# Performance work log

Measured on AMD Instinct MI355X. Metric: run time of the kernel, lower is better.

The kernel has to match this reference:

```python
import jax, jax.numpy as jnp
import numpy as np

S, B, H = 4096, 1, 2048       # [seq, batch, hidden] layout (NeoX convention)
NP, HN = 16, H // 16          # heads, head dim
ROT = int(HN * 0.25)          # rotary_ndims = 32 (rotary_pct=0.25)
ROPE_BASE = 10000.0


def setup_inputs() -> dict:
    key = jax.random.key(0)
    k0, k1, k2 = jax.random.split(key, 3)
    hidden_states = jax.random.normal(k0, (S, B, H), jnp.float32) * 0.02
    # causal left-to-right mask: True = masked out (filled with -10000)
    attention_mask = jnp.triu(jnp.ones((1, 1, S, S), bool), k=1)
    w_qkv = jax.random.normal(k1, (3 * H, H), jnp.float32) * (1.0 / np.sqrt(H))
    w_dense = jax.random.normal(k2, (H, H), jnp.float32) * (1.0 / np.sqrt(H))
    b_dense = jnp.zeros((H,), jnp.float32)
    return {"hidden_states": hidden_states, "attention_mask": attention_mask,
            "w_qkv": w_qkv, "w_dense": w_dense, "b_dense": b_dense}


def _apply_rope(x, pos):
    # x: [s, b, np, ROT]; NeoX rotate_half convention
    inv_freq = 1.0 / (ROPE_BASE ** (jnp.arange(0, ROT, 2, dtype=jnp.float32) / ROT))
    freqs = pos[:, None] * inv_freq[None, :]              # [s, ROT/2]
    emb = jnp.concatenate([freqs, freqs], axis=-1)        # [s, ROT]
    cos = jnp.cos(emb)[:, None, None, :]
    sin = jnp.sin(emb)[:, None, None, :]
    x1, x2 = jnp.split(x, 2, axis=-1)
    rot = jnp.concatenate([-x2, x1], axis=-1)
    return x * cos + rot * sin


def reference(hidden_states, attention_mask, w_qkv, w_dense, b_dense):
    s, b, h = hidden_states.shape
    # fused QKV projection (no bias), reshape to [s, b, np, 3*hn], split
    qkv = (hidden_states @ w_qkv.T).reshape(s, b, NP, 3 * HN)
    q, k, v = jnp.split(qkv, 3, axis=-1)                  # each [s, b, np, hn]
    # partial rotary embedding on first ROT dims
    pos = jnp.arange(s, dtype=jnp.float32)
    q = jnp.concatenate([_apply_rope(q[..., :ROT], pos), q[..., ROT:]], axis=-1)
    k = jnp.concatenate([_apply_rope(k[..., :ROT], pos), k[..., ROT:]], axis=-1)
    # raw attention scores [b, np, s_q, s_k], scale 1/sqrt(hn)
    scores = jnp.einsum('sbhd,tbhd->bhst', q, k) / np.float32(np.sqrt(HN))
    # ltor mask: fill masked positions with -10000, softmax in fp32
    scores = jnp.where(attention_mask, jnp.float32(-10000.0), scores)
    probs = jax.nn.softmax(scores.astype(jnp.float32), axis=-1).astype(hidden_states.dtype)
    # context [s, b, np, hn] -> [s, b, h]
    ctx = jnp.einsum('bhst,tbhd->sbhd', probs, v).reshape(s, b, h)
    return ctx @ w_dense.T + b_dense
```

## Files before the change

### kernel.cpp

```cpp
#include <hip/hip_runtime.h>

#define S_LEN 4096
#define HID   2048
#define NHEAD 16
#define HDIM  128
#define QSCALE_L2E 0.12751664352f

typedef float  f32x4  __attribute__((ext_vector_type(4)));
typedef float  f32x16 __attribute__((ext_vector_type(16)));
typedef __bf16 bf16x8 __attribute__((ext_vector_type(8)));
typedef unsigned u32x4 __attribute__((ext_vector_type(4)));
typedef unsigned u32x2 __attribute__((ext_vector_type(2)));

#define MFMA16(a, b, c) __builtin_amdgcn_mfma_f32_16x16x32_bf16((a), (b), (c), 0, 0, 0)
#define MFMA32(a, b, c) __builtin_amdgcn_mfma_f32_32x32x16_bf16((a), (b), (c), 0, 0, 0)

__device__ __forceinline__ void gld16(const void* g, void* l) {
  __builtin_amdgcn_global_load_lds(
      (const __attribute__((address_space(1))) void*)(unsigned long long)(g),
      (__attribute__((address_space(3))) void*)(unsigned long long)(l),
      16, 0, 0);
}

__device__ __forceinline__ unsigned short f2bf(float f) {
  union { float f; unsigned u; } v; v.f = f;
  unsigned r = v.u + 0x7FFFu + ((v.u >> 16) & 1u);
  return (unsigned short)(r >> 16);
}
__device__ __forceinline__ float bf2f(unsigned short h) {
  union { unsigned u; float f; } v; v.u = ((unsigned)h) << 16;
  return v.f;
}
__device__ __forceinline__ unsigned cvtpk_bf16(float a, float b) {
  unsigned r;
  asm("v_cvt_pk_bf16_f32 %0, %1, %2" : "=v"(r) : "v"(a), "v"(b));
  return r;
}
__device__ __forceinline__ u32x2 pls(unsigned a, unsigned b) {
  return __builtin_amdgcn_permlane32_swap(a, b, false, false);
}
__device__ __forceinline__ float asf(unsigned u) { return __builtin_bit_cast(float, u); }
__device__ __forceinline__ unsigned asu(float f) { return __builtin_bit_cast(unsigned, f); }

__global__ __launch_bounds__(256) void cvt_kernel(const float* __restrict__ src,
                                                  unsigned short* __restrict__ dst, int n) {
  int i = (blockIdx.x * 256 + threadIdx.x) * 4;
  if (i >= n) return;
  const float4 v = *(const float4*)(src + i);
  ushort4 o;
  o.x = f2bf(v.x); o.y = f2bf(v.y); o.z = f2bf(v.z); o.w = f2bf(v.w);
  *(ushort4*)(dst + i) = o;
}

__global__ __launch_bounds__(256, 3) void gemm_qkv_kernel(
    const unsigned short* __restrict__ A, const unsigned short* __restrict__ B,
    unsigned short* __restrict__ Qb, unsigned short* __restrict__ Kb,
    unsigned short* __restrict__ Vt) {
  __shared__ __align__(16) unsigned short As[2][128 * 32];
  __shared__ __align__(16) unsigned short Bs[2][128 * 32];
  const int K = HID;
  const int bid = ((int)blockIdx.x % 8) * 192 + (int)blockIdx.x / 8;
  const int bm = bid / 48, bn = bid % 48;
  const int row0 = bm * 128, col0 = bn * 128;
  const int tid = threadIdx.x;
  const int wid = tid >> 6, lane = tid & 63;
  const int g = lane >> 4, r16 = lane & 15;
  const int wr = wid >> 1, wc = wid & 1;

  f32x4 acc[4][4] = {};

  int srow[2], scol[2];
#pragma unroll
  for (int c = 0; c < 2; ++c) {
    int byteoff = (wid * 2 + c) * 1024 + lane * 16;
    srow[c] = byteoff >> 6;
    scol[c] = (byteoff & 63) >> 1;
  }

  auto stage = [&](int buf, int t) {
    const int k0 = t * 32;
#pragma unroll
    for (int c = 0; c < 2; ++c) {
      gld16(A + (row0 + srow[c]) * K + k0 + scol[c], &As[buf][(wid * 2 + c) * 512]);
      gld16(B + (col0 + srow[c]) * K + k0 + scol[c], &Bs[buf][(wid * 2 + c) * 512]);
    }
  };

  const int nt = K / 32;
  stage(0, 0);
  __syncthreads();
  for (int t = 0; t < nt; ++t) {
    const int cur = t & 1;
    if (t + 1 < nt) stage(cur ^ 1, t + 1);
    const char* as = (const char*)As[cur];
    const char* bs = (const char*)Bs[cur];
    bf16x8 af[4], bfv[4];
#pragma unroll
    for (int m = 0; m < 4; ++m)
      af[m] = *(const bf16x8*)(as + (wr * 64 + m * 16 + r16) * 64 + g * 16);
#pragma unroll
    for (int n = 0; n < 4; ++n)
      bfv[n] = *(const bf16x8*)(bs + (wc * 64 + n * 16 + r16) * 64 + g * 16);
#pragma unroll
    for (int m = 0; m < 4; ++m)
#pragma unroll
      for (int n = 0; n < 4; ++n)
        acc[m][n] = MFMA16(af[m], bfv[n], acc[m][n]);
    __syncthreads();
  }

  const int type = bn % 3, p = bn / 3;
#pragma unroll
  for (int m = 0; m < 4; ++m) {
    const int s0 = row0 + wr * 64 + m * 16 + g * 4;
#pragma unroll
    for (int n = 0; n < 4; ++n) {
      const int d = wc * 64 + n * 16 + r16;
      if (type == 0) {
#pragma unroll
        for (int r = 0; r < 4; ++r)
          Qb[(p * S_LEN + s0 + r) * HDIM + d] = f2bf(acc[m][n][r] * QSCALE_L2E);
      } else if (type == 1) {
#pragma unroll
        for (int r = 0; r < 4; ++r)
          Kb[(p * S_LEN + s0 + r) * HDIM + d] = f2bf(acc[m][n][r]);
      } else {
        ushort4 o;
        o.x = f2bf(acc[m][n][0]); o.y = f2bf(acc[m][n][1]);
        o.z = f2bf(acc[m][n][2]); o.w = f2bf(acc[m][n][3]);
        *(ushort4*)(Vt + (p * HDIM + d) * S_LEN + s0) = o;
      }
    }
  }
}

__global__ __launch_bounds__(256) void rope_kernel(unsigned short* __restrict__ Qb,
                                                   unsigned short* __restrict__ Kb) {
  const int idx = blockIdx.x * 256 + threadIdx.x;
  const int p = idx >> 16, rem = idx & 65535, s = rem >> 4, d = rem & 15;
  const float invf = exp2f(-(float)d * (13.287712379549449f / 16.0f));
  const float ang = (float)s * invf;
  const float c = cosf(ang), sn = sinf(ang);
  const int base = (p * S_LEN + s) * HDIM;
  {
    float x = bf2f(Qb[base + d]), y = bf2f(Qb[base + d + 16]);
    Qb[base + d]      = f2bf(x * c - y * sn);
    Qb[base + d + 16] = f2bf(y * c + x * sn);
  }
  {
    float x = bf2f(Kb[base + d]), y = bf2f(Kb[base + d + 16]);
    Kb[base + d]      = f2bf(x * c - y * sn);
    Kb[base + d + 16] = f2bf(y * c + x * sn);
  }
}

__global__ __launch_bounds__(256, 2) void attn_kernel(
    const unsigned short* __restrict__ Qb, const unsigned short* __restrict__ Kb,
    const unsigned short* __restrict__ Vt, unsigned short* __restrict__ Ctx) {
  __shared__ __align__(16) unsigned char sm[65536];
  unsigned char* const Kl0 = sm;
  unsigned char* const Vl0 = sm + 32768;
  const int b = (int)blockIdx.x;
  const int p = b & 15;
  const int qt = (b < 256) ? (b >> 4) : 47 - (b >> 4);
  const int tid = threadIdx.x, wid = tid >> 6, lane = tid & 63;
  const int l31 = lane & 31, hi = lane >> 5;
  const int xr = (l31 & 7) << 4;

  auto stageKV = [&](int buf, int t) {
    const unsigned short* kb = Kb + (p * S_LEN + t * 64) * HDIM;
    const unsigned short* vb = Vt + p * HDIM * S_LEN + t * 64;
#pragma unroll
    for (int c = 0; c < 4; ++c) {
      const int chunk = c * 256 + tid;
      const int byteoff = chunk * 16;
      {
        const int j = byteoff >> 8, cb = (byteoff >> 4) & 15;
        gld16(kb + j * HDIM + (cb ^ (j & 7)) * 8, Kl0 + buf * 16384 + chunk * 16);
      }
      {
        const int dd = byteoff >> 7, cb = (byteoff >> 4) & 7;
        gld16(vb + dd * S_LEN + (cb ^ (dd & 7)) * 8, Vl0 + buf * 16384 + chunk * 16);
      }
    }
  };

  const int q0w = qt * 128 + wid * 32;
  const int qg = q0w + l31;
  const int nt = 2 * (qt + 1);

  stageKV(0, 0);
  bf16x8 qf[8];
  {
    const unsigned short* qp_ = Qb + (p * S_LEN + qg) * HDIM + hi * 8;
#pragma unroll
    for (int dd = 0; dd < 8; ++dd) qf[dd] = *(const bf16x8*)(qp_ + dd * 16);
  }
  f32x16 acc[4] = {};
  float m_s = -1e30f, l_s = 0.f;

  __syncthreads();
  for (int t = 0; t < nt; ++t) {
    const int cur = t & 1;
    if (t + 1 < nt) stageKV(cur ^ 1, t + 1);
    const unsigned char* kl = Kl0 + cur * 16384;
    const unsigned char* vl = Vl0 + cur * 16384;

    f32x16 sv0 = {}, sv1 = {};
    __builtin_amdgcn_s_setprio(1);
#pragma unroll
    for (int dd = 0; dd < 8; ++dd) {
      bf16x8 k0 = *(const bf16x8*)(kl + l31 * 256 + (((dd * 2 + hi) << 4) ^ xr));
      bf16x8 k1 = *(const bf16x8*)(kl + (32 + l31) * 256 + (((dd * 2 + hi) << 4) ^ xr));
      sv0 = MFMA32(k0, qf[dd], sv0);
      sv1 = MFMA32(k1, qf[dd], sv1);
    }
    __builtin_amdgcn_s_setprio(0);
    if (t * 64 + 63 > q0w) {
#pragma unroll
      for (int r = 0; r < 16; ++r) {
        const int kv0 = t * 64 + ((r & 3) + 8 * (r >> 2)) + 4 * hi;
        if (kv0 > qg) sv0[r] = -1e30f;
        if (kv0 + 32 > qg) sv1[r] = -1e30f;
      }
    }
    float mx[16];
#pragma unroll
    for (int r = 0; r < 16; ++r) mx[r] = fmaxf(sv0[r], sv1[r]);
#pragma unroll
    for (int r = 0; r < 8; ++r) mx[r] = fmaxf(mx[r], mx[r + 8]);
#pragma unroll
    for (int r = 0; r < 4; ++r) mx[r] = fmaxf(mx[r], mx[r + 4]);
    mx[0] = fmaxf(fmaxf(mx[0], mx[2]), fmaxf(mx[1], mx[3]));
    float pm;
    {
      u32x2 e = pls(asu(mx[0]), asu(mx[0]));
      pm = fmaxf(asf(e.x), asf(e.y));
    }
    if (__any(pm > m_s + 11.5f)) {
      const float mn = fmaxf(m_s, pm);
      const float scl = exp2f(m_s - mn);
#pragma unroll
      for (int d32 = 0; d32 < 4; ++d32)
#pragma unroll
        for (int r = 0; r < 16; ++r) acc[d32][r] *= scl;
      l_s *= scl;
      m_s = mn;
    }
#pragma unroll
    for (int r = 0; r < 16; ++r) {
      sv0[r] = exp2f(sv0[r] - m_s);
      sv1[r] = exp2f(sv1[r] - m_s);
    }
    {
      float s_[8];
#pragma unroll
      for (int r = 0; r < 8; ++r) s_[r] = (sv0[r] + sv0[r + 8]) + (sv1[r] + sv1[r + 8]);
#pragma unroll
      for (int r = 0; r < 4; ++r) s_[r] += s_[r + 4];
      const float rs = (s_[0] + s_[1]) + (s_[2] + s_[3]);
      u32x2 e = pls(asu(rs), asu(rs));
      l_s += asf(e.x) + asf(e.y);
    }
    bf16x8 pf[4];
#define PACKB(B, SV, base)                                                        \
    {                                                                             \
      unsigned X0 = cvtpk_bf16(SV[base + 0], SV[base + 1]);                       \
      unsigned X1 = cvtpk_bf16(SV[base + 2], SV[base + 3]);                       \
      unsigned Y0 = cvtpk_bf16(SV[base + 4], SV[base + 5]);                       \
      unsigned Y1 = cvtpk_bf16(SV[base + 6], SV[base + 7]);                       \
      u32x2 e0 = pls(X0, Y0);                                                     \
      u32x2 e1 = pls(X1, Y1);                                                     \
      u32x4 pw;                                                                   \
      pw.x = e0.x; pw.y = e1.x; pw.z = e0.y; pw.w = e1.y;                         \
      pf[B] = __builtin_bit_cast(bf16x8, pw);                                     \
    }
    PACKB(0, sv0, 0)
    PACKB(1, sv0, 8)
    PACKB(2, sv1, 0)
    PACKB(3, sv1, 8)
#undef PACKB
    __builtin_amdgcn_s_setprio(1);
#pragma unroll
    for (int d32 = 0; d32 < 4; ++d32) {
#pragma unroll
      for (int bb = 0; bb < 4; ++bb) {
        bf16x8 vf = *(const bf16x8*)(vl + (d32 * 32 + l31) * 128 + (((bb * 2 + hi) << 4) ^ xr));
        acc[d32] = MFMA32(vf, pf[bb], acc[d32]);
      }
    }
    __builtin_amdgcn_s_setprio(0);
    __syncthreads();
  }
  const float inv = 1.0f / l_s;
  unsigned short* cbase = Ctx + qg * HID + p * HDIM;
#pragma unroll
  for (int d32 = 0; d32 < 4; ++d32)
#pragma unroll
    for (int r = 0; r < 16; ++r) {
      const int d = d32 * 32 + ((r & 3) + 8 * (r >> 2)) + 4 * hi;
      cbase[d] = f2bf(acc[d32][r] * inv);
    }
}

__global__ __launch_bounds__(256, 3) void gemm_dense_kernel(
    const unsigned short* __restrict__ A, const unsigned short* __restrict__ B,
    const float* __restrict__ bias, float* __restrict__ out) {
  __shared__ __align__(16) unsigned short As[2][128 * 32];
  __shared__ __align__(16) unsigned short Bs[2][128 * 32];
  const int K = HID;
  const int bid = ((int)blockIdx.x % 8) * 64 + (int)blockIdx.x / 8;
  const int bm = bid / 16, bn = bid % 16;
  const int row0 = bm * 128, col0 = bn * 128;
  const int tid = threadIdx.x;
  const int wid = tid >> 6, lane = tid & 63;
  const int g = lane >> 4, r16 = lane & 15;
  const int wr = wid >> 1, wc = wid & 1;

  f32x4 acc[4][4] = {};

  int srow[2], scol[2];
#pragma unroll
  for (int c = 0; c < 2; ++c) {
    int byteoff = (wid * 2 + c) * 1024 + lane * 16;
    srow[c] = byteoff >> 6;
    scol[c] = (byteoff & 63) >> 1;
  }
  auto stage = [&](int buf, int t) {
    const int k0 = t * 32;
#pragma unroll
    for (int c = 0; c < 2; ++c) {
      gld16(A + (row0 + srow[c]) * K + k0 + scol[c], &As[buf][(wid * 2 + c) * 512]);
      gld16(B + (col0 + srow[c]) * K + k0 + scol[c], &Bs[buf][(wid * 2 + c) * 512]);
    }
  };

  const int nt = K / 32;
  stage(0, 0);
  __syncthreads();
  for (int t = 0; t < nt; ++t) {
    const int cur = t & 1;
    if (t + 1 < nt) stage(cur ^ 1, t + 1);
    const char* as = (const char*)As[cur];
    const char* bs = (const char*)Bs[cur];
    bf16x8 af[4], bfv[4];
#pragma unroll
    for (int m = 0; m < 4; ++m)
      af[m] = *(const bf16x8*)(as + (wr * 64 + m * 16 + r16) * 64 + g * 16);
#pragma unroll
    for (int n = 0; n < 4; ++n)
      bfv[n] = *(const bf16x8*)(bs + (wc * 64 + n * 16 + r16) * 64 + g * 16);
#pragma unroll
    for (int m = 0; m < 4; ++m)
#pragma unroll
      for (int n = 0; n < 4; ++n)
        acc[m][n] = MFMA16(af[m], bfv[n], acc[m][n]);
    __syncthreads();
  }

#pragma unroll
  for (int m = 0; m < 4; ++m) {
    const int s0 = row0 + wr * 64 + m * 16 + g * 4;
#pragma unroll
    for (int n = 0; n < 4; ++n) {
      const int col = col0 + wc * 64 + n * 16 + r16;
      const float bv = bias[col];
#pragma unroll
      for (int r = 0; r < 4; ++r)
        out[(s0 + r) * HID + col] = acc[m][n][r] + bv;
    }
  }
}

extern "C" void kernel_launch(void* const* d_in, const int* in_sizes, int n_in,
                              void* d_out, int out_size, void* d_ws, size_t ws_size,
                              hipStream_t stream) {
  (void)in_sizes; (void)n_in; (void)out_size; (void)ws_size;
  const float* hidden = (const float*)d_in[0];
  const float* wqkv   = (const float*)d_in[2];
  const float* wdense = (const float*)d_in[3];
  const float* bdense = (const float*)d_in[4];
  float* out = (float*)d_out;

  char* ws = (char*)d_ws;
  unsigned short* hiddenB = (unsigned short*)(ws);
  unsigned short* wqkvB   = (unsigned short*)(ws + 16777216);
  unsigned short* wdenseB = (unsigned short*)(ws + 41943040);
  unsigned short* Qb      = (unsigned short*)(ws + 50331648);
  unsigned short* Kb      = (unsigned short*)(ws + 67108864);
  unsigned short* Vt      = (unsigned short*)(ws + 83886080);
  unsigned short* ctxB    = (unsigned short*)(ws + 100663296);

  cvt_kernel<<<8192, 256, 0, stream>>>(hidden, hiddenB, 8388608);
  cvt_kernel<<<12288, 256, 0, stream>>>(wqkv, wqkvB, 12582912);
  cvt_kernel<<<4096, 256, 0, stream>>>(wdense, wdenseB, 4194304);
  gemm_qkv_kernel<<<1536, 256, 0, stream>>>(hiddenB, wqkvB, Qb, Kb, Vt);
  rope_kernel<<<4096, 256, 0, stream>>>(Qb, Kb);
  attn_kernel<<<512, 256, 0, stream>>>(Qb, Kb, Vt, ctxB);
  gemm_dense_kernel<<<512, 256, 0, stream>>>(ctxB, wdenseB, bdense, out);
}
```

Baseline: 339.7 us.

## Software-pipeline attention loop: overlap next tile's QK with current softmax/PV

Restructures the flash-attention main loop into a two-tile software pipeline. The QK^T MFMAs for the next KV tile are issued before the softmax and PV of the current tile, so matrix work can overlap the exp and reduction VALU work. K uses two LDS slots and V uses a rotating triple buffer, which raises shared memory from 64KB to 80KB. The row-sum reduction also moves after the PV MFMAs. Extra live score registers and the larger LDS footprint may reduce occupancy at the requested two blocks per CU.

```diff
diff --git a/kernel.cpp b/kernel.cpp
--- a/kernel.cpp
+++ b/kernel.cpp
@@ -157,9 +157,7 @@
 __global__ __launch_bounds__(256, 2) void attn_kernel(
     const unsigned short* __restrict__ Qb, const unsigned short* __restrict__ Kb,
     const unsigned short* __restrict__ Vt, unsigned short* __restrict__ Ctx) {
-  __shared__ __align__(16) unsigned char sm[65536];
-  unsigned char* const Kl0 = sm;
-  unsigned char* const Vl0 = sm + 32768;
+  __shared__ __align__(16) unsigned char sm[81920];
   const int b = (int)blockIdx.x;
   const int p = b & 15;
   const int qt = (b < 256) ? (b >> 4) : 47 - (b >> 4);
@@ -167,66 +165,54 @@
   const int l31 = lane & 31, hi = lane >> 5;
   const int xr = (l31 & 7) << 4;
 
-  auto stageKV = [&](int buf, int t) {
+  const int q0w = qt * 128 + wid * 32;
+  const int qg = q0w + l31;
+  const int nt = 2 * (qt + 1);
+  const int np = nt >> 1;
+
+  auto stage = [&](int t, int ko, int vo) {
     const unsigned short* kb = Kb + (p * S_LEN + t * 64) * HDIM;
     const unsigned short* vb = Vt + p * HDIM * S_LEN + t * 64;
 #pragma unroll
     for (int c = 0; c < 4; ++c) {
       const int chunk = c * 256 + tid;
       const int byteoff = chunk * 16;
-      {
-        const int j = byteoff >> 8, cb = (byteoff >> 4) & 15;
-        gld16(kb + j * HDIM + (cb ^ (j & 7)) * 8, Kl0 + buf * 16384 + chunk * 16);
-      }
-      {
-        const int dd = byteoff >> 7, cb = (byteoff >> 4) & 7;
-        gld16(vb + dd * S_LEN + (cb ^ (dd & 7)) * 8, Vl0 + buf * 16384 + chunk * 16);
-      }
+      const int j = byteoff >> 8, cbK = (byteoff >> 4) & 15;
+      gld16(kb + j * HDIM + (cbK ^ (j & 7)) * 8, sm + ko + chunk * 16);
+      const int dd = byteoff >> 7, cbV = (byteoff >> 4) & 7;
+      gld16(vb + dd * S_LEN + (cbV ^ (dd & 7)) * 8, sm + vo + chunk * 16);
     }
   };
 
-  const int q0w = qt * 128 + wid * 32;
-  const int qg = q0w + l31;
-  const int nt = 2 * (qt + 1);
-
-  stageKV(0, 0);
   bf16x8 qf[8];
-  {
-    const unsigned short* qp_ = Qb + (p * S_LEN + qg) * HDIM + hi * 8;
-#pragma unroll
-    for (int dd = 0; dd < 8; ++dd) qf[dd] = *(const bf16x8*)(qp_ + dd * 16);
-  }
   f32x16 acc[4] = {};
   float m_s = -1e30f, l_s = 0.f;
 
-  __syncthreads();
-  for (int t = 0; t < nt; ++t) {
-    const int cur = t & 1;
-    if (t + 1 < nt) stageKV(cur ^ 1, t + 1);
-    const unsigned char* kl = Kl0 + cur * 16384;
-    const unsigned char* vl = Vl0 + cur * 16384;
-
-    f32x16 sv0 = {}, sv1 = {};
+  auto qk = [&](f32x16& s0, f32x16& s1, const unsigned char* kl) {
     __builtin_amdgcn_s_setprio(1);
 #pragma unroll
     for (int dd = 0; dd < 8; ++dd) {
       bf16x8 k0 = *(const bf16x8*)(kl + l31 * 256 + (((dd * 2 + hi) << 4) ^ xr));
       bf16x8 k1 = *(const bf16x8*)(kl + (32 + l31) * 256 + (((dd * 2 + hi) << 4) ^ xr));
-      sv0 = MFMA32(k0, qf[dd], sv0);
-      sv1 = MFMA32(k1, qf[dd], sv1);
+      s0 = MFMA32(k0, qf[dd], s0);
+      s1 = MFMA32(k1, qf[dd], s1);
     }
     __builtin_amdgcn_s_setprio(0);
+  };
+
+  auto smpv = [&](f32x16& s0, f32x16& s1, int t, int vo) {
+    const unsigned char* vl = sm + vo;
     if (t * 64 + 63 > q0w) {
 #pragma unroll
       for (int r = 0; r < 16; ++r) {
         const int kv0 = t * 64 + ((r & 3) + 8 * (r >> 2)) + 4 * hi;
-        if (kv0 > qg) sv0[r] = -1e30f;
-        if (kv0 + 32 > qg) sv1[r] = -1e30f;
+        if (kv0 > qg) s0[r] = -1e30f;
+        if (kv0 + 32 > qg) s1[r] = -1e30f;
       }
     }
     float mx[16];
 #pragma unroll
-    for (int r = 0; r < 16; ++r) mx[r] = fmaxf(sv0[r], sv1[r]);
+    for (int r = 0; r < 16; ++r) mx[r] = fmaxf(s0[r], s1[r]);
 #pragma unroll
     for (int r = 0; r < 8; ++r) mx[r] = fmaxf(mx[r], mx[r + 8]);
 #pragma unroll
@@ -249,18 +235,8 @@
     }
 #pragma unroll
     for (int r = 0; r < 16; ++r) {
-      sv0[r] = exp2f(sv0[r] - m_s);
-      sv1[r] = exp2f(sv1[r] - m_s);
-    }
-    {
-      float s_[8];
-#pragma unroll
-      for (int r = 0; r < 8; ++r) s_[r] = (sv0[r] + sv0[r + 8]) + (sv1[r] + sv1[r + 8]);
-#pragma unroll
-      for (int r = 0; r < 4; ++r) s_[r] += s_[r + 4];
-      const float rs = (s_[0] + s_[1]) + (s_[2] + s_[3]);
-      u32x2 e = pls(asu(rs), asu(rs));
-      l_s += asf(e.x) + asf(e.y);
+      s0[r] = exp2f(s0[r] - m_s);
+      s1[r] = exp2f(s1[r] - m_s);
     }
     bf16x8 pf[4];
 #define PACKB(B, SV, base)                                                        \
@@ -275,10 +251,10 @@
       pw.x = e0.x; pw.y = e1.x; pw.z = e0.y; pw.w = e1.y;                         \
       pf[B] = __builtin_bit_cast(bf16x8, pw);                                     \
     }
-    PACKB(0, sv0, 0)
-    PACKB(1, sv0, 8)
-    PACKB(2, sv1, 0)
-    PACKB(3, sv1, 8)
+    PACKB(0, s0, 0)
+    PACKB(1, s0, 8)
+    PACKB(2, s1, 0)
+    PACKB(3, s1, 8)
 #undef PACKB
     __builtin_amdgcn_s_setprio(1);
 #pragma unroll
@@ -290,8 +266,48 @@
       }
     }
     __builtin_amdgcn_s_setprio(0);
+    float s_[8];
+#pragma unroll
+    for (int r = 0; r < 8; ++r) s_[r] = (s0[r] + s0[r + 8]) + (s1[r] + s1[r + 8]);
+#pragma unroll
+    for (int r = 0; r < 4; ++r) s_[r] += s_[r + 4];
+    const float rs = (s_[0] + s_[1]) + (s_[2] + s_[3]);
+    u32x2 e = pls(asu(rs), asu(rs));
+    l_s += asf(e.x) + asf(e.y);
+  };
+
+  stage(0, 0, 32768);
+  stage(1, 16384, 49152);
+  {
+    const unsigned short* qp_ = Qb + (p * S_LEN + qg) * HDIM + hi * 8;
+#pragma unroll
+    for (int dd = 0; dd < 8; ++dd) qf[dd] = *(const bf16x8*)(qp_ + dd * 16);
+  }
+  int vcur = 32768, vnext = 49152, vstage = 65536;
+  __syncthreads();
+  f32x16 sA0 = {}, sA1 = {};
+  qk(sA0, sA1, sm);
+  __syncthreads();
+
+  for (int tt = 0; tt < np; ++tt) {
+    const bool more = (tt + 1 < np);
+    const int t = 2 * tt;
+    f32x16 sB0 = {}, sB1 = {};
+    qk(sB0, sB1, sm + 16384);
+    if (more) stage(t + 2, 0, vstage);
+    smpv(sA0, sA1, t, vcur);
+    { int tmp = vcur; vcur = vnext; vnext = vstage; vstage = tmp; }
     __syncthreads();
-  }
+    if (more) {
+      sA0 = {}; sA1 = {};
+      qk(sA0, sA1, sm);
+      stage(t + 3, 16384, vstage);
+    }
+    smpv(sB0, sB1, t + 1, vcur);
+    { int tmp = vcur; vcur = vnext; vnext = vstage; vstage = tmp; }
+    __syncthreads();
+  }
+
   const float inv = 1.0f / l_s;
   unsigned short* cbase = Ctx + qg * HID + p * HDIM;
 #pragma unroll
```

After: 331.0 us. 1.03x faster.
